# Kernel tuning notes

Measured on AMD Instinct MI355X. Metric: run time of the kernel, lower is better.

Reference implementation:

```python
import jax, jax.numpy as jnp
import numpy as np

WS, SS, NH = 7, 3, 4  # window_size, shift_size, num_heads


def _rel_position_index(wh, ww):
    # torch doublestepseq: seq1 step (2*Ww-1) len Wh, seq2 step 1 len Ww
    seq1 = np.arange(wh) * (2 * ww - 1)
    seq2 = np.arange(ww)
    rel = (seq1[:, None] + seq2[None, :]).reshape(1, -1)  # [1, Wh*Ww]
    idx = rel + rel.T                                      # [N, N]
    return np.ascontiguousarray(idx[:, ::-1])              # flip dim 1


def _shift_mask(hp, wp, ws, ss):
    img = np.zeros((hp, wp))
    cnt = 0
    sls = (slice(0, -ws), slice(-ws, -ss), slice(-ss, None))
    for h in sls:
        for w in sls:
            img[h, w] = cnt
            cnt += 1
    mw = img.reshape(hp // ws, ws, wp // ws, ws).transpose(0, 2, 1, 3).reshape(-1, ws * ws)
    diff = mw[:, None, :] - mw[:, :, None]  # [nW, N, N]
    return np.where(diff != 0, -100.0, 0.0).astype(np.float32)


def setup_inputs() -> dict:
    key = jax.random.key(0)
    ks = jax.random.split(key, 6)
    B, H, W, C = 64, 56, 56, 128
    return {
        "query": jax.random.normal(ks[0], (B, H * W, C), jnp.float32),
        "rpb_table": jax.random.normal(ks[1], ((2 * WS - 1) ** 2, NH), jnp.float32) * 0.02,
        "qkv_w": jax.random.normal(ks[2], (3 * C, C), jnp.float32) * (C ** -0.5),
        "qkv_b": jax.random.normal(ks[3], (3 * C,), jnp.float32) * 0.02,
        "proj_w": jax.random.normal(ks[4], (C, C), jnp.float32) * (C ** -0.5),
        "proj_b": jax.random.normal(ks[5], (C,), jnp.float32) * 0.02,
        "H": H,
        "W": W,
    }


def reference(query, rpb_table, qkv_w, qkv_b, proj_w, proj_b, H, W):
    B, L, C = query.shape
    hd = C // NH
    N = WS * WS
    x = query.reshape(B, H, W, C)
    pad_b, pad_r = (-H) % WS, (-W) % WS
    x = jnp.pad(x, ((0, 0), (0, pad_b), (0, pad_r), (0, 0)))
    Hp, Wp = H + pad_b, W + pad_r
    nW = (Hp // WS) * (Wp // WS)
    # cyclic shift
    x = jnp.roll(x, (-SS, -SS), axis=(1, 2))
    # window partition -> [B*nW, N, C]
    xw = x.reshape(B, Hp // WS, WS, Wp // WS, WS, C).transpose(0, 1, 3, 2, 4, 5).reshape(-1, N, C)
    nB = xw.shape[0]
    qkv = (xw @ qkv_w.T + qkv_b).reshape(nB, N, 3, NH, hd).transpose(2, 0, 3, 1, 4)
    q, k, v = qkv[0] * (hd ** -0.5), qkv[1], qkv[2]
    attn = jnp.einsum("bhnd,bhmd->bhnm", q, k)  # [nB, NH, N, N]
    rel_idx = _rel_position_index(WS, WS)
    bias = rpb_table[rel_idx.reshape(-1)].reshape(N, N, NH).transpose(2, 0, 1)
    attn = attn + bias[None]
    mask = jnp.asarray(_shift_mask(Hp, Wp, WS, SS))  # [nW, N, N]
    attn = (attn.reshape(B, nW, NH, N, N) + mask[None, :, None]).reshape(nB, NH, N, N)
    attn = jax.nn.softmax(attn, axis=-1)
    out = jnp.einsum("bhnm,bhmd->bhnd", attn, v).transpose(0, 2, 1, 3).reshape(nB, N, C)
    out = out @ proj_w.T + proj_b
    # window reverse
    out = out.reshape(B, Hp // WS, Wp // WS, WS, WS, C).transpose(0, 1, 3, 2, 4, 5).reshape(B, Hp, Wp, C)
    out = jnp.roll(out, (SS, SS), axis=(1, 2))[:, :H, :W, :]
    return out.reshape(B, H * W, C)
```

## Files before the change

### kernel.cpp

```cpp
#include <hip/hip_runtime.h>
#include <hip/hip_bf16.h>

typedef short s16x8 __attribute__((ext_vector_type(8)));
typedef short s16x4 __attribute__((ext_vector_type(4)));
typedef float f32x4 __attribute__((ext_vector_type(4)));
typedef unsigned short u16;

namespace {

constexpr int NHEAD = 4;
constexpr int CDIM  = 128;
constexpr int NTOK  = 49;
constexpr int IMG   = 56;
constexpr int NWIN  = 4096;
constexpr float QSCALE = 0.17677669529663687f;

__device__ inline u16 f2bf(float x) {
  union { __hip_bfloat16 b; u16 u; } cv;
  cv.b = __float2bfloat16(x);
  return cv.u;
}
__device__ inline float bf2f(u16 h) { return __uint_as_float(((unsigned)h) << 16); }
__device__ inline int div7(int t) { return (t * 9363) >> 16; }

__device__ inline f32x4 mfma32(s16x8 a, s16x8 b, f32x4 c) {
  return __builtin_amdgcn_mfma_f32_16x16x32_bf16(a, b, c, 0, 0, 0);
}
__device__ inline f32x4 mfma16(s16x4 a, s16x4 b, f32x4 c) {
#if __has_builtin(__builtin_amdgcn_mfma_f32_16x16x16bf16_1k)
  return __builtin_amdgcn_mfma_f32_16x16x16bf16_1k(a, b, c, 0, 0, 0);
#else
  f32x4 d;
  asm volatile("v_mfma_f32_16x16x16_bf16 %0, %1, %2, %3"
               : "=v"(d) : "v"(a), "v"(b), "v"(c));
  return d;
#endif
}
__device__ inline s16x4 pack4(f32x4 v) {
  s16x4 r;
  r[0] = (short)f2bf(v[0]); r[1] = (short)f2bf(v[1]);
  r[2] = (short)f2bf(v[2]); r[3] = (short)f2bf(v[3]);
  return r;
}

__global__ void prep(const float* __restrict__ qkvw, const float* __restrict__ projw,
                     const float* __restrict__ rpb,
                     u16* __restrict__ wq, u16* __restrict__ wp, u16* __restrict__ btab) {
  int i = blockIdx.x * 256 + threadIdx.x;
  if (i < 384 * 128) wq[i] = f2bf(qkvw[i]);
  if (i < 128 * 128) wp[i] = f2bf(projw[i]);
  if (i < 65536) {
    int m = i & 63, n = (i >> 6) & 63, h = (i >> 12) & 3, cls = (i >> 14) & 3;
    float v;
    if (m >= NTOK) v = -1e9f;
    else if (n >= NTOK) v = 0.f;
    else {
      int tin = div7(n), tjn = n - tin * 7;
      int tim = div7(m), tjm = m - tim * 7;
      int ridx = 13 * (tin - tim + 6) + (tjn - tjm + 6);
      v = rpb[ridx * NHEAD + h];
      int wy = (cls & 2) ? 7 : 0, wx = (cls & 1) ? 7 : 0;
      int mhn = wy * 7 + tin, mwn = wx * 7 + tjn;
      int mhm = wy * 7 + tim, mwm = wx * 7 + tjm;
      int cn = ((mhn < 49) ? 0 : ((mhn < 53) ? 1 : 2)) * 3 + ((mwn < 49) ? 0 : ((mwn < 53) ? 1 : 2));
      int cm = ((mhm < 49) ? 0 : ((mhm < 53) ? 1 : 2)) * 3 + ((mwm < 49) ? 0 : ((mwm < 53) ? 1 : 2));
      if (cn != cm) v -= 100.f;
    }
    btab[i] = f2bf(v);
  }
}

__global__ __launch_bounds__(64, 2) void swin_wave(
    const float* __restrict__ xin,
    const float* __restrict__ qkvb,
    const float* __restrict__ projb,
    const u16*  __restrict__ wq,
    const u16*  __restrict__ wp,
    const u16*  __restrict__ btab,
    float* __restrict__ outp)
{
  const int wb = blockIdx.x;
  const int bb = wb >> 6, wy = (wb >> 3) & 7, wx = wb & 7;
  const int lane = threadIdx.x;
  const int g = lane >> 4, lj = lane & 15;
  const int cls = ((wy == 7) ? 2 : 0) | ((wx == 7) ? 1 : 0);

  auto gposf = [&](int tok) -> int {
    int t  = (tok < NTOK) ? tok : 0;
    int ti = div7(t), tj = t - ti * 7;
    int gh = wy * 7 + ti + 3; if (gh >= IMG) gh -= IMG;
    int gw = wx * 7 + tj + 3; if (gw >= IMG) gw -= IMG;
    return gh * IMG + gw;
  };

  const float* xb = xin + (size_t)bb * (IMG * IMG * CDIM);
  s16x8 X[4][4];
  #pragma unroll
  for (int mt = 0; mt < 4; ++mt) {
    int tok = 16 * mt + lj;
    bool ok = tok < NTOK;
    const float* xr = xb + (size_t)gposf(tok) * CDIM;
    #pragma unroll
    for (int ks = 0; ks < 4; ++ks) {
      s16x8 r = {0, 0, 0, 0, 0, 0, 0, 0};
      if (ok) {
        float4 a = *reinterpret_cast<const float4*>(xr + 32 * ks + 8 * g);
        float4 b = *reinterpret_cast<const float4*>(xr + 32 * ks + 8 * g + 4);
        r[0] = (short)f2bf(a.x); r[1] = (short)f2bf(a.y);
        r[2] = (short)f2bf(a.z); r[3] = (short)f2bf(a.w);
        r[4] = (short)f2bf(b.x); r[5] = (short)f2bf(b.y);
        r[6] = (short)f2bf(b.z); r[7] = (short)f2bf(b.w);
      }
      X[mt][ks] = r;
    }
  }

  s16x4 oa[4][8];

  #pragma unroll
  for (int h = 0; h < NHEAD; ++h) {
    s16x4 Kbf[4][2];
    #pragma unroll
    for (int dt = 0; dt < 2; ++dt) {
      s16x8 wa[4];
      #pragma unroll
      for (int ks = 0; ks < 4; ++ks)
        wa[ks] = *reinterpret_cast<const s16x8*>(
            &wq[(size_t)(128 + 32 * h + 16 * dt + lj) * 128 + 32 * ks + 8 * g]);
      f32x4 bk4 = *reinterpret_cast<const f32x4*>(&qkvb[128 + 32 * h + 16 * dt + 4 * g]);
      #pragma unroll
      for (int mt = 0; mt < 4; ++mt) {
        f32x4 c = {0.f, 0.f, 0.f, 0.f};
        #pragma unroll
        for (int ks = 0; ks < 4; ++ks) c = mfma32(wa[ks], X[mt][ks], c);
        Kbf[mt][dt] = pack4(c + bk4);
      }
    }
    s16x4 Qbf[2][4];
    #pragma unroll
    for (int dt = 0; dt < 2; ++dt) {
      s16x8 wa[4];
      #pragma unroll
      for (int ks = 0; ks < 4; ++ks)
        wa[ks] = *reinterpret_cast<const s16x8*>(
            &wq[(size_t)(32 * h + 16 * dt + lj) * 128 + 32 * ks + 8 * g]);
      f32x4 bq4 = *reinterpret_cast<const f32x4*>(&qkvb[32 * h + 16 * dt + 4 * g]);
      #pragma unroll
      for (int nt = 0; nt < 4; ++nt) {
        f32x4 c = {0.f, 0.f, 0.f, 0.f};
        #pragma unroll
        for (int ks = 0; ks < 4; ++ks) c = mfma32(wa[ks], X[nt][ks], c);
        f32x4 q;
        #pragma unroll
        for (int r2 = 0; r2 < 4; ++r2) q[r2] = (c[r2] + bq4[r2]) * QSCALE;
        Qbf[dt][nt] = pack4(q);
      }
    }
    s16x4 Vbf[4][2];
    #pragma unroll
    for (int dt = 0; dt < 2; ++dt) {
      s16x8 wbv[4];
      #pragma unroll
      for (int ks = 0; ks < 4; ++ks)
        wbv[ks] = *reinterpret_cast<const s16x8*>(
            &wq[(size_t)(256 + 32 * h + 16 * dt + lj) * 128 + 32 * ks + 8 * g]);
      float bv = qkvb[256 + 32 * h + 16 * dt + lj];
      #pragma unroll
      for (int mt = 0; mt < 4; ++mt) {
        f32x4 c = {0.f, 0.f, 0.f, 0.f};
        #pragma unroll
        for (int ks = 0; ks < 4; ++ks) c = mfma32(X[mt][ks], wbv[ks], c);
        f32x4 v;
        #pragma unroll
        for (int r2 = 0; r2 < 4; ++r2) v[r2] = c[r2] + bv;
        Vbf[mt][dt] = pack4(v);
      }
    }
    const u16* bt = btab + (((cls << 2) + h) << 12);
    #pragma unroll
    for (int nt = 0; nt < 4; ++nt) {
      f32x4 st[4];
      #pragma unroll
      for (int mt = 0; mt < 4; ++mt) {
        f32x4 c = mfma16(Kbf[mt][0], Qbf[0][nt], (f32x4){0.f, 0.f, 0.f, 0.f});
        c = mfma16(Kbf[mt][1], Qbf[1][nt], c);
        s16x4 bb4 = *reinterpret_cast<const s16x4*>(&bt[((16 * nt + lj) << 6) + 16 * mt + 4 * g]);
        #pragma unroll
        for (int r2 = 0; r2 < 4; ++r2) c[r2] += bf2f((u16)bb4[r2]);
        st[mt] = c;
      }
      float mx = -3e38f;
      #pragma unroll
      for (int mt = 0; mt < 4; ++mt)
        #pragma unroll
        for (int r2 = 0; r2 < 4; ++r2) mx = fmaxf(mx, st[mt][r2]);
      mx = fmaxf(mx, __shfl_xor(mx, 16, 64));
      mx = fmaxf(mx, __shfl_xor(mx, 32, 64));
      float sm = 0.f;
      #pragma unroll
      for (int mt = 0; mt < 4; ++mt)
        #pragma unroll
        for (int r2 = 0; r2 < 4; ++r2) {
          float e = __expf(st[mt][r2] - mx);
          st[mt][r2] = e;
          sm += e;
        }
      sm += __shfl_xor(sm, 16, 64);
      sm += __shfl_xor(sm, 32, 64);
      float inv = 1.f / sm;
      s16x4 Pt[4];
      #pragma unroll
      for (int mt = 0; mt < 4; ++mt) {
        f32x4 p;
        #pragma unroll
        for (int r2 = 0; r2 < 4; ++r2) p[r2] = st[mt][r2] * inv;
        Pt[mt] = pack4(p);
      }
      #pragma unroll
      for (int dt = 0; dt < 2; ++dt) {
        f32x4 oc = {0.f, 0.f, 0.f, 0.f};
        #pragma unroll
        for (int mt = 0; mt < 4; ++mt) oc = mfma16(Vbf[mt][dt], Pt[mt], oc);
        oa[nt][2 * h + dt] = pack4(oc);
      }
    }
  }

  int gp[4][4];
  bool tv[4][4];
  #pragma unroll
  for (int nt = 0; nt < 4; ++nt)
    #pragma unroll
    for (int r2 = 0; r2 < 4; ++r2) {
      int tok = 16 * nt + 4 * g + r2;
      gp[nt][r2] = gposf(tok);
      tv[nt][r2] = tok < NTOK;
    }
  float* ob = outp + (size_t)bb * (IMG * IMG * CDIM);
  #pragma unroll 1
  for (int ct = 0; ct < 8; ++ct) {
    s16x4 wpb[8];
    #pragma unroll
    for (int kp = 0; kp < 8; ++kp)
      wpb[kp] = *reinterpret_cast<const s16x4*>(
          &wp[(size_t)(16 * ct + lj) * 128 + 16 * kp + 4 * g]);
    float bias = projb[16 * ct + lj];
    #pragma unroll
    for (int nt = 0; nt < 4; ++nt) {
      f32x4 y = {0.f, 0.f, 0.f, 0.f};
      #pragma unroll
      for (int kp = 0; kp < 8; ++kp) y = mfma16(oa[nt][kp], wpb[kp], y);
      #pragma unroll
      for (int r2 = 0; r2 < 4; ++r2)
        if (tv[nt][r2])
          ob[(size_t)gp[nt][r2] * CDIM + 16 * ct + lj] = y[r2] + bias;
    }
  }
}

}

extern "C" void kernel_launch(void* const* d_in, const int* in_sizes, int n_in,
                              void* d_out, int out_size, void* d_ws, size_t ws_size,
                              hipStream_t stream) {
  const float* x     = (const float*)d_in[0];
  const float* rpb   = (const float*)d_in[1];
  const float* qkvw  = (const float*)d_in[2];
  const float* qkvb  = (const float*)d_in[3];
  const float* projw = (const float*)d_in[4];
  const float* projb = (const float*)d_in[5];
  u16* wq   = (u16*)d_ws;
  u16* wp   = wq + 384 * 128;
  u16* btab = wp + 128 * 128;

  prep<<<256, 256, 0, stream>>>(qkvw, projw, rpb, wq, wp, btab);
  swin_wave<<<NWIN, 64, 0, stream>>>(x, qkvb, projb, wq, wp, btab, (float*)d_out);
}
```

Before: 151.1 us.

## Split heads across four waves per window and exchange outputs via LDS

Each window block now uses four waves, one per attention head, instead of one wave looping over all heads. Per-head attention outputs are written to a swizzled shared-memory buffer, then after a barrier each wave computes the output projection for one 16-token tile. This increases parallelism and cuts per-wave register use. In exchange, every wave reloads and converts the input window, adding a barrier and LDS traffic.

```diff
diff --git a/kernel.cpp b/kernel.cpp
--- a/kernel.cpp
+++ b/kernel.cpp
@@ -70,7 +70,11 @@
   }
 }
 
-__global__ __launch_bounds__(64, 2) void swin_wave(
+__device__ inline int adr128(int r, int c) {
+  return r * 128 + (c & 7) + 8 * (((c >> 3) ^ (r & 7)) & 15);
+}
+
+__global__ __launch_bounds__(256, 3) void swin_wave(
     const float* __restrict__ xin,
     const float* __restrict__ qkvb,
     const float* __restrict__ projb,
@@ -79,9 +83,12 @@
     const u16*  __restrict__ btab,
     float* __restrict__ outp)
 {
+  __shared__ u16 o_lds[8192];
+
   const int wb = blockIdx.x;
   const int bb = wb >> 6, wy = (wb >> 3) & 7, wx = wb & 7;
-  const int lane = threadIdx.x;
+  const int h    = threadIdx.x >> 6;
+  const int lane = threadIdx.x & 63;
   const int g = lane >> 4, lj = lane & 15;
   const int cls = ((wy == 7) ? 2 : 0) | ((wx == 7) ? 1 : 0);
 
@@ -115,146 +122,144 @@
     }
   }
 
-  s16x4 oa[4][8];
-
-  #pragma unroll
-  for (int h = 0; h < NHEAD; ++h) {
-    s16x4 Kbf[4][2];
+  s16x4 Kbf[4][2];
+  #pragma unroll
+  for (int dt = 0; dt < 2; ++dt) {
+    s16x8 wa[4];
+    #pragma unroll
+    for (int ks = 0; ks < 4; ++ks)
+      wa[ks] = *reinterpret_cast<const s16x8*>(
+          &wq[(size_t)(128 + 32 * h + 16 * dt + lj) * 128 + 32 * ks + 8 * g]);
+    f32x4 bk4 = *reinterpret_cast<const f32x4*>(&qkvb[128 + 32 * h + 16 * dt + 4 * g]);
+    #pragma unroll
+    for (int mt = 0; mt < 4; ++mt) {
+      f32x4 c = {0.f, 0.f, 0.f, 0.f};
+      #pragma unroll
+      for (int ks = 0; ks < 4; ++ks) c = mfma32(wa[ks], X[mt][ks], c);
+      Kbf[mt][dt] = pack4(c + bk4);
+    }
+  }
+  s16x4 Qbf[2][4];
+  #pragma unroll
+  for (int dt = 0; dt < 2; ++dt) {
+    s16x8 wa[4];
+    #pragma unroll
+    for (int ks = 0; ks < 4; ++ks)
+      wa[ks] = *reinterpret_cast<const s16x8*>(
+          &wq[(size_t)(32 * h + 16 * dt + lj) * 128 + 32 * ks + 8 * g]);
+    f32x4 bq4 = *reinterpret_cast<const f32x4*>(&qkvb[32 * h + 16 * dt + 4 * g]);
+    #pragma unroll
+    for (int nt = 0; nt < 4; ++nt) {
+      f32x4 c = {0.f, 0.f, 0.f, 0.f};
+      #pragma unroll
+      for (int ks = 0; ks < 4; ++ks) c = mfma32(wa[ks], X[nt][ks], c);
+      f32x4 q;
+      #pragma unroll
+      for (int r2 = 0; r2 < 4; ++r2) q[r2] = (c[r2] + bq4[r2]) * QSCALE;
+      Qbf[dt][nt] = pack4(q);
+    }
+  }
+  s16x4 Vbf[4][2];
+  #pragma unroll
+  for (int dt = 0; dt < 2; ++dt) {
+    s16x8 wbv[4];
+    #pragma unroll
+    for (int ks = 0; ks < 4; ++ks)
+      wbv[ks] = *reinterpret_cast<const s16x8*>(
+          &wq[(size_t)(256 + 32 * h + 16 * dt + lj) * 128 + 32 * ks + 8 * g]);
+    float bv = qkvb[256 + 32 * h + 16 * dt + lj];
+    #pragma unroll
+    for (int mt = 0; mt < 4; ++mt) {
+      f32x4 c = {0.f, 0.f, 0.f, 0.f};
+      #pragma unroll
+      for (int ks = 0; ks < 4; ++ks) c = mfma32(X[mt][ks], wbv[ks], c);
+      f32x4 v;
+      #pragma unroll
+      for (int r2 = 0; r2 < 4; ++r2) v[r2] = c[r2] + bv;
+      Vbf[mt][dt] = pack4(v);
+    }
+  }
+
+  const u16* bt = btab + (((cls << 2) + h) << 12);
+  #pragma unroll
+  for (int nt = 0; nt < 4; ++nt) {
+    f32x4 st[4];
+    #pragma unroll
+    for (int mt = 0; mt < 4; ++mt) {
+      f32x4 c = mfma16(Kbf[mt][0], Qbf[0][nt], (f32x4){0.f, 0.f, 0.f, 0.f});
+      c = mfma16(Kbf[mt][1], Qbf[1][nt], c);
+      s16x4 bb4 = *reinterpret_cast<const s16x4*>(&bt[((16 * nt + lj) << 6) + 16 * mt + 4 * g]);
+      #pragma unroll
+      for (int r2 = 0; r2 < 4; ++r2) c[r2] += bf2f((u16)bb4[r2]);
+      st[mt] = c;
+    }
+    float mx = -3e38f;
+    #pragma unroll
+    for (int mt = 0; mt < 4; ++mt)
+      #pragma unroll
+      for (int r2 = 0; r2 < 4; ++r2) mx = fmaxf(mx, st[mt][r2]);
+    mx = fmaxf(mx, __shfl_xor(mx, 16, 64));
+    mx = fmaxf(mx, __shfl_xor(mx, 32, 64));
+    float sm = 0.f;
+    #pragma unroll
+    for (int mt = 0; mt < 4; ++mt)
+      #pragma unroll
+      for (int r2 = 0; r2 < 4; ++r2) {
+        float e = __expf(st[mt][r2] - mx);
+        st[mt][r2] = e;
+        sm += e;
+      }
+    sm += __shfl_xor(sm, 16, 64);
+    sm += __shfl_xor(sm, 32, 64);
+    float inv = 1.f / sm;
+    s16x4 Pt[4];
+    #pragma unroll
+    for (int mt = 0; mt < 4; ++mt) {
+      f32x4 p;
+      #pragma unroll
+      for (int r2 = 0; r2 < 4; ++r2) p[r2] = st[mt][r2] * inv;
+      Pt[mt] = pack4(p);
+    }
     #pragma unroll
     for (int dt = 0; dt < 2; ++dt) {
-      s16x8 wa[4];
-      #pragma unroll
-      for (int ks = 0; ks < 4; ++ks)
-        wa[ks] = *reinterpret_cast<const s16x8*>(
-            &wq[(size_t)(128 + 32 * h + 16 * dt + lj) * 128 + 32 * ks + 8 * g]);
-      f32x4 bk4 = *reinterpret_cast<const f32x4*>(&qkvb[128 + 32 * h + 16 * dt + 4 * g]);
-      #pragma unroll
-      for (int mt = 0; mt < 4; ++mt) {
-        f32x4 c = {0.f, 0.f, 0.f, 0.f};
-        #pragma unroll
-        for (int ks = 0; ks < 4; ++ks) c = mfma32(wa[ks], X[mt][ks], c);
-        Kbf[mt][dt] = pack4(c + bk4);
-      }
-    }
-    s16x4 Qbf[2][4];
-    #pragma unroll
-    for (int dt = 0; dt < 2; ++dt) {
-      s16x8 wa[4];
-      #pragma unroll
-      for (int ks = 0; ks < 4; ++ks)
-        wa[ks] = *reinterpret_cast<const s16x8*>(
-            &wq[(size_t)(32 * h + 16 * dt + lj) * 128 + 32 * ks + 8 * g]);
-      f32x4 bq4 = *reinterpret_cast<const f32x4*>(&qkvb[32 * h + 16 * dt + 4 * g]);
-      #pragma unroll
-      for (int nt = 0; nt < 4; ++nt) {
-        f32x4 c = {0.f, 0.f, 0.f, 0.f};
-        #pragma unroll
-        for (int ks = 0; ks < 4; ++ks) c = mfma32(wa[ks], X[nt][ks], c);
-        f32x4 q;
-        #pragma unroll
-        for (int r2 = 0; r2 < 4; ++r2) q[r2] = (c[r2] + bq4[r2]) * QSCALE;
-        Qbf[dt][nt] = pack4(q);
-      }
-    }
-    s16x4 Vbf[4][2];
-    #pragma unroll
-    for (int dt = 0; dt < 2; ++dt) {
-      s16x8 wbv[4];
-      #pragma unroll
-      for (int ks = 0; ks < 4; ++ks)
-        wbv[ks] = *reinterpret_cast<const s16x8*>(
-            &wq[(size_t)(256 + 32 * h + 16 * dt + lj) * 128 + 32 * ks + 8 * g]);
-      float bv = qkvb[256 + 32 * h + 16 * dt + lj];
-      #pragma unroll
-      for (int mt = 0; mt < 4; ++mt) {
-        f32x4 c = {0.f, 0.f, 0.f, 0.f};
-        #pragma unroll
-        for (int ks = 0; ks < 4; ++ks) c = mfma32(X[mt][ks], wbv[ks], c);
-        f32x4 v;
-        #pragma unroll
-        for (int r2 = 0; r2 < 4; ++r2) v[r2] = c[r2] + bv;
-        Vbf[mt][dt] = pack4(v);
-      }
-    }
-    const u16* bt = btab + (((cls << 2) + h) << 12);
-    #pragma unroll
-    for (int nt = 0; nt < 4; ++nt) {
-      f32x4 st[4];
-      #pragma unroll
-      for (int mt = 0; mt < 4; ++mt) {
-        f32x4 c = mfma16(Kbf[mt][0], Qbf[0][nt], (f32x4){0.f, 0.f, 0.f, 0.f});
-        c = mfma16(Kbf[mt][1], Qbf[1][nt], c);
-        s16x4 bb4 = *reinterpret_cast<const s16x4*>(&bt[((16 * nt + lj) << 6) + 16 * mt + 4 * g]);
-        #pragma unroll
-        for (int r2 = 0; r2 < 4; ++r2) c[r2] += bf2f((u16)bb4[r2]);
-        st[mt] = c;
-      }
-      float mx = -3e38f;
-      #pragma unroll
-      for (int mt = 0; mt < 4; ++mt)
-        #pragma unroll
-        for (int r2 = 0; r2 < 4; ++r2) mx = fmaxf(mx, st[mt][r2]);
-      mx = fmaxf(mx, __shfl_xor(mx, 16, 64));
-      mx = fmaxf(mx, __shfl_xor(mx, 32, 64));
-      float sm = 0.f;
-      #pragma unroll
-      for (int mt = 0; mt < 4; ++mt)
-        #pragma unroll
-        for (int r2 = 0; r2 < 4; ++r2) {
-          float e = __expf(st[mt][r2] - mx);
-          st[mt][r2] = e;
-          sm += e;
-        }
-      sm += __shfl_xor(sm, 16, 64);
-      sm += __shfl_xor(sm, 32, 64);
-      float inv = 1.f / sm;
-      s16x4 Pt[4];
-      #pragma unroll
-      for (int mt = 0; mt < 4; ++mt) {
-        f32x4 p;
-        #pragma unroll
-        for (int r2 = 0; r2 < 4; ++r2) p[r2] = st[mt][r2] * inv;
-        Pt[mt] = pack4(p);
-      }
-      #pragma unroll
-      for (int dt = 0; dt < 2; ++dt) {
-        f32x4 oc = {0.f, 0.f, 0.f, 0.f};
-        #pragma unroll
-        for (int mt = 0; mt < 4; ++mt) oc = mfma16(Vbf[mt][dt], Pt[mt], oc);
-        oa[nt][2 * h + dt] = pack4(oc);
-      }
-    }
-  }
-
-  int gp[4][4];
-  bool tv[4][4];
-  #pragma unroll
-  for (int nt = 0; nt < 4; ++nt)
-    #pragma unroll
-    for (int r2 = 0; r2 < 4; ++r2) {
-      int tok = 16 * nt + 4 * g + r2;
-      gp[nt][r2] = gposf(tok);
-      tv[nt][r2] = tok < NTOK;
-    }
+      f32x4 oc = {0.f, 0.f, 0.f, 0.f};
+      #pragma unroll
+      for (int mt = 0; mt < 4; ++mt) oc = mfma16(Vbf[mt][dt], Pt[mt], oc);
+      *reinterpret_cast<s16x4*>(
+          &o_lds[adr128(16 * nt + lj, 32 * h + 16 * dt + 4 * g)]) = pack4(oc);
+    }
+  }
+  __syncthreads();
+
+  const int nt = h;
+  s16x4 oa[8];
+  #pragma unroll
+  for (int kp = 0; kp < 8; ++kp)
+    oa[kp] = *reinterpret_cast<const s16x4*>(&o_lds[adr128(16 * nt + lj, 16 * kp + 4 * g)]);
+  int gp[4];
+  bool tv[4];
+  #pragma unroll
+  for (int r2 = 0; r2 < 4; ++r2) {
+    int tok = 16 * nt + 4 * g + r2;
+    gp[r2] = gposf(tok);
+    tv[r2] = tok < NTOK;
+  }
   float* ob = outp + (size_t)bb * (IMG * IMG * CDIM);
-  #pragma unroll 1
+  #pragma unroll
   for (int ct = 0; ct < 8; ++ct) {
     s16x4 wpb[8];
     #pragma unroll
     for (int kp = 0; kp < 8; ++kp)
       wpb[kp] = *reinterpret_cast<const s16x4*>(
           &wp[(size_t)(16 * ct + lj) * 128 + 16 * kp + 4 * g]);
+    f32x4 y = {0.f, 0.f, 0.f, 0.f};
+    #pragma unroll
+    for (int kp = 0; kp < 8; ++kp) y = mfma16(oa[kp], wpb[kp], y);
     float bias = projb[16 * ct + lj];
     #pragma unroll
-    for (int nt = 0; nt < 4; ++nt) {
-      f32x4 y = {0.f, 0.f, 0.f, 0.f};
-      #pragma unroll
-      for (int kp = 0; kp < 8; ++kp) y = mfma16(oa[nt][kp], wpb[kp], y);
-      #pragma unroll
-      for (int r2 = 0; r2 < 4; ++r2)
-        if (tv[nt][r2])
-          ob[(size_t)gp[nt][r2] * CDIM + 16 * ct + lj] = y[r2] + bias;
-    }
+    for (int r2 = 0; r2 < 4; ++r2)
+      if (tv[r2])
+        ob[(size_t)gp[r2] * CDIM + 16 * ct + lj] = y[r2] + bias;
   }
 }
 
@@ -274,5 +279,5 @@
   u16* btab = wp + 128 * 128;
 
   prep<<<256, 256, 0, stream>>>(qkvw, projw, rpb, wq, wp, btab);
-  swin_wave<<<NWIN, 64, 0, stream>>>(x, qkvb, projb, wq, wp, btab, (float*)d_out);
-}
+  swin_wave<<<NWIN, 256, 0, stream>>>(x, qkvb, projb, wq, wp, btab, (float*)d_out);
+}
```

New measurement: 253.3 us. +67.7%, slower.

## Stage bf16 input window in swizzled LDS to free registers, raise occupancy

Applied to the files above, without the earlier changes.

The converted bf16 window tile used to sit in 64 VGPRs per lane. It now lives in a 16 KB shared-memory buffer with an XOR-swizzled layout and is re-read for each Q/K/V MFMA. Launch bounds go from 2 to 4 waves per EU so more blocks can be resident and hide global-load latency. The cost is repeated LDS reads inside the projection loops and 16 KB of LDS per single-wave block, which may itself limit residency.

```diff
diff --git a/kernel.cpp b/kernel.cpp
--- a/kernel.cpp
+++ b/kernel.cpp
@@ -70,7 +70,11 @@
   }
 }
 
-__global__ __launch_bounds__(64, 2) void swin_wave(
+__device__ inline int adr128(int r, int c) {
+  return r * 128 + (c & 7) + 8 * (((c >> 3) ^ (r & 7)) & 15);
+}
+
+__global__ __launch_bounds__(64, 4) void swin_wave(
     const float* __restrict__ xin,
     const float* __restrict__ qkvb,
     const float* __restrict__ projb,
@@ -79,6 +83,8 @@
     const u16*  __restrict__ btab,
     float* __restrict__ outp)
 {
+  __shared__ u16 X_lds[8192];
+
   const int wb = blockIdx.x;
   const int bb = wb >> 6, wy = (wb >> 3) & 7, wx = wb & 7;
   const int lane = threadIdx.x;
@@ -93,25 +99,27 @@
     return gh * IMG + gw;
   };
 
-  const float* xb = xin + (size_t)bb * (IMG * IMG * CDIM);
-  s16x8 X[4][4];
-  #pragma unroll
-  for (int mt = 0; mt < 4; ++mt) {
-    int tok = 16 * mt + lj;
-    bool ok = tok < NTOK;
-    const float* xr = xb + (size_t)gposf(tok) * CDIM;
-    #pragma unroll
-    for (int ks = 0; ks < 4; ++ks) {
-      s16x8 r = {0, 0, 0, 0, 0, 0, 0, 0};
-      if (ok) {
-        float4 a = *reinterpret_cast<const float4*>(xr + 32 * ks + 8 * g);
-        float4 b = *reinterpret_cast<const float4*>(xr + 32 * ks + 8 * g + 4);
-        r[0] = (short)f2bf(a.x); r[1] = (short)f2bf(a.y);
-        r[2] = (short)f2bf(a.z); r[3] = (short)f2bf(a.w);
-        r[4] = (short)f2bf(b.x); r[5] = (short)f2bf(b.y);
-        r[6] = (short)f2bf(b.z); r[7] = (short)f2bf(b.w);
-      }
-      X[mt][ks] = r;
+  {
+    const float* xb = xin + (size_t)bb * (IMG * IMG * CDIM);
+    #pragma unroll
+    for (int mt = 0; mt < 4; ++mt) {
+      int row = 16 * mt + lj;
+      bool ok = row < NTOK;
+      const float* xr = xb + (size_t)gposf(row) * CDIM;
+      #pragma unroll
+      for (int G = 0; G < 4; ++G) {
+        int c0 = 32 * G + 8 * g;
+        s16x8 r = {0, 0, 0, 0, 0, 0, 0, 0};
+        if (ok) {
+          float4 a = *reinterpret_cast<const float4*>(xr + c0);
+          float4 b = *reinterpret_cast<const float4*>(xr + c0 + 4);
+          r[0] = (short)f2bf(a.x); r[1] = (short)f2bf(a.y);
+          r[2] = (short)f2bf(a.z); r[3] = (short)f2bf(a.w);
+          r[4] = (short)f2bf(b.x); r[5] = (short)f2bf(b.y);
+          r[6] = (short)f2bf(b.z); r[7] = (short)f2bf(b.w);
+        }
+        *reinterpret_cast<s16x8*>(&X_lds[adr128(row, c0)]) = r;
+      }
     }
   }
 
@@ -127,13 +135,17 @@
       for (int ks = 0; ks < 4; ++ks)
         wa[ks] = *reinterpret_cast<const s16x8*>(
             &wq[(size_t)(128 + 32 * h + 16 * dt + lj) * 128 + 32 * ks + 8 * g]);
-      f32x4 bk4 = *reinterpret_cast<const f32x4*>(&qkvb[128 + 32 * h + 16 * dt + 4 * g]);
+      f32x4 bk = *reinterpret_cast<const f32x4*>(&qkvb[128 + 32 * h + 16 * dt + 4 * g]);
       #pragma unroll
       for (int mt = 0; mt < 4; ++mt) {
         f32x4 c = {0.f, 0.f, 0.f, 0.f};
         #pragma unroll
-        for (int ks = 0; ks < 4; ++ks) c = mfma32(wa[ks], X[mt][ks], c);
-        Kbf[mt][dt] = pack4(c + bk4);
+        for (int ks = 0; ks < 4; ++ks) {
+          s16x8 Xf = *reinterpret_cast<const s16x8*>(
+              &X_lds[adr128(16 * mt + lj, 32 * ks + 8 * g)]);
+          c = mfma32(wa[ks], Xf, c);
+        }
+        Kbf[mt][dt] = pack4(c + bk);
       }
     }
     s16x4 Qbf[2][4];
@@ -144,15 +156,19 @@
       for (int ks = 0; ks < 4; ++ks)
         wa[ks] = *reinterpret_cast<const s16x8*>(
             &wq[(size_t)(32 * h + 16 * dt + lj) * 128 + 32 * ks + 8 * g]);
-      f32x4 bq4 = *reinterpret_cast<const f32x4*>(&qkvb[32 * h + 16 * dt + 4 * g]);
+      f32x4 bq = *reinterpret_cast<const f32x4*>(&qkvb[32 * h + 16 * dt + 4 * g]);
       #pragma unroll
       for (int nt = 0; nt < 4; ++nt) {
         f32x4 c = {0.f, 0.f, 0.f, 0.f};
         #pragma unroll
-        for (int ks = 0; ks < 4; ++ks) c = mfma32(wa[ks], X[nt][ks], c);
+        for (int ks = 0; ks < 4; ++ks) {
+          s16x8 Xf = *reinterpret_cast<const s16x8*>(
+              &X_lds[adr128(16 * nt + lj, 32 * ks + 8 * g)]);
+          c = mfma32(wa[ks], Xf, c);
+        }
         f32x4 q;
         #pragma unroll
-        for (int r2 = 0; r2 < 4; ++r2) q[r2] = (c[r2] + bq4[r2]) * QSCALE;
+        for (int r2 = 0; r2 < 4; ++r2) q[r2] = (c[r2] + bq[r2]) * QSCALE;
         Qbf[dt][nt] = pack4(q);
       }
     }
@@ -169,13 +185,18 @@
       for (int mt = 0; mt < 4; ++mt) {
         f32x4 c = {0.f, 0.f, 0.f, 0.f};
         #pragma unroll
-        for (int ks = 0; ks < 4; ++ks) c = mfma32(X[mt][ks], wbv[ks], c);
+        for (int ks = 0; ks < 4; ++ks) {
+          s16x8 Xf = *reinterpret_cast<const s16x8*>(
+              &X_lds[adr128(16 * mt + lj, 32 * ks + 8 * g)]);
+          c = mfma32(Xf, wbv[ks], c);
+        }
         f32x4 v;
         #pragma unroll
         for (int r2 = 0; r2 < 4; ++r2) v[r2] = c[r2] + bv;
         Vbf[mt][dt] = pack4(v);
       }
     }
+
     const u16* bt = btab + (((cls << 2) + h) << 12);
     #pragma unroll
     for (int nt = 0; nt < 4; ++nt) {
```

Result: no change. 151.4 us (median of 2 runs) (+0.2%).
